# Optimization experiments

Hardware: AMD Instinct MI355X
Metric: run time of the kernel (lower is better)

Reference implementation:

```python
import jax, jax.numpy as jnp
import numpy as np

B, H, W, DIM, WS, SHIFT, HEADS = 32, 56, 56, 256, 7, 3, 8
N = WS * WS          # 49 tokens per window
C2 = 2 * DIM         # concatenated two-modal channel dim
NW = (H // WS) * (W // WS)


def _rel_index(ws):
    coords = np.stack(np.meshgrid(np.arange(ws), np.arange(ws), indexing='ij')).reshape(2, -1)
    rel = (coords[:, :, None] - coords[:, None, :]).transpose(1, 2, 0)
    rel[:, :, 0] += ws - 1
    rel[:, :, 1] += ws - 1
    rel[:, :, 0] *= 2 * ws - 1
    return rel.sum(-1)  # (N, N) int

REL_IDX = _rel_index(WS).reshape(-1)


def _attn_mask():
    # standard Swin shifted-window mask: 0 / -100 per window pair
    img = np.zeros((H, W))
    cnt = 0
    for hs in (slice(0, H - WS), slice(H - WS, H - SHIFT), slice(H - SHIFT, H)):
        for ws_ in (slice(0, W - WS), slice(W - WS, W - SHIFT), slice(W - SHIFT, W)):
            img[hs, ws_] = cnt
            cnt += 1
    mw = img.reshape(H // WS, WS, W // WS, WS).transpose(0, 2, 1, 3).reshape(-1, N)
    d = mw[:, None, :] - mw[:, :, None]
    return np.where(d != 0, -100.0, 0.0).astype(np.float32)  # (nW, N, N)

ATTN_MASK = _attn_mask()


def _win_part(x):  # (B,H,W,C) -> (nW*B, N, C)
    b, c = x.shape[0], x.shape[-1]
    x = x.reshape(b, H // WS, WS, W // WS, WS, c).transpose(0, 1, 3, 2, 4, 5)
    return x.reshape(-1, N, c)


def _win_rev(w, b):  # (nW*B, N, C) -> (B,H,W,C)
    c = w.shape[-1]
    x = w.reshape(b, H // WS, W // WS, WS, WS, c).transpose(0, 1, 3, 2, 4, 5)
    return x.reshape(b, H, W, c)


def _ln(t, g, bb):
    m = t.mean(-1, keepdims=True)
    v = t.var(-1, keepdims=True)
    return (t - m) / jnp.sqrt(v + 1e-5) * g + bb


def setup_inputs() -> dict:
    key = jax.random.key(0)
    ks = jax.random.split(key, 8)
    def nrm(k, shape, s=0.02):
        return jax.random.normal(k, shape, jnp.float32) * s
    return {
        'x': jax.random.normal(ks[0], (B, H * W, DIM), jnp.float32),
        'y': jax.random.normal(ks[1], (B, H * W, DIM), jnp.float32),
        'g1': jnp.ones((DIM,), jnp.float32), 'b1': jnp.zeros((DIM,), jnp.float32),
        'rpb': nrm(ks[2], ((2 * WS - 1) * (2 * WS - 1), HEADS)),
        'w_qkv': nrm(ks[3], (6 * DIM, 2 * DIM)), 'b_qkv': jnp.zeros((6 * DIM,), jnp.float32),
        'w_proj': nrm(ks[4], (DIM, 2 * DIM)), 'b_proj': jnp.zeros((DIM,), jnp.float32),
        'g2': jnp.ones((DIM,), jnp.float32), 'b2': jnp.zeros((DIM,), jnp.float32),
        'w_fc1': nrm(ks[5], (4 * DIM, DIM)), 'b_fc1': jnp.zeros((4 * DIM,), jnp.float32),
        'w_fc2': nrm(ks[6], (DIM, 4 * DIM)), 'b_fc2': jnp.zeros((DIM,), jnp.float32),
    }


def reference(x, y, g1, b1, rpb, w_qkv, b_qkv, w_proj, b_proj, g2, b2, w_fc1, b_fc1, w_fc2, b_fc2):
    scale = (DIM // HEADS) ** -0.5  # as in __init__: head_dim = dim // num_heads
    shortcut = x
    xn = _ln(x, g1, b1).reshape(B, H, W, DIM)
    yn = _ln(y, g1, b1).reshape(B, H, W, DIM)
    # cyclic shift
    xn = jnp.roll(xn, (-SHIFT, -SHIFT), axis=(1, 2))
    yn = jnp.roll(yn, (-SHIFT, -SHIFT), axis=(1, 2))
    xw, yw = _win_part(xn), _win_part(yn)            # (nW*B, N, C)
    xy = jnp.concatenate([xw, yw], axis=-1)          # (nW*B, N, 2C)
    nwb, hd = xy.shape[0], C2 // HEADS
    qkv = (xy @ w_qkv.T + b_qkv).reshape(nwb, N, 3, HEADS, hd).transpose(2, 0, 3, 1, 4)
    q, k, v = qkv[0] * scale, qkv[1], qkv[2]         # (nW*B, h, N, d)
    attn = jnp.einsum('whnd,whmd->whnm', q, k)
    bias = rpb[REL_IDX].reshape(N, N, HEADS).transpose(2, 0, 1)  # (h, N, N)
    attn = attn + bias[None]
    attn = attn.reshape(B, NW, HEADS, N, N) + jnp.asarray(ATTN_MASK)[None, :, None]
    attn = jax.nn.softmax(attn.reshape(nwb, HEADS, N, N), axis=-1)
    out = jnp.einsum('whnm,whmd->whnd', attn, v).transpose(0, 2, 1, 3).reshape(nwb, N, C2)
    out = out @ w_proj.T + b_proj                    # fuse 2C -> C
    out = _win_rev(out, B)
    out = jnp.roll(out, (SHIFT, SHIFT), axis=(1, 2)).reshape(B, H * W, DIM)
    x = shortcut + out
    h = _ln(x, g2, b2)
    h = jax.nn.gelu(h @ w_fc1.T + b_fc1, approximate=False)
    return x + h @ w_fc2.T + b_fc2
```

## Files before the change

kernel.cpp:

```cpp
#include <hip/hip_runtime.h>
#include <hip/hip_bf16.h>

#define DEVI __device__ __forceinline__

typedef __attribute__((ext_vector_type(8))) short short8;
typedef __attribute__((ext_vector_type(4))) float f32x4;
typedef unsigned int u32;
typedef unsigned short u16;

typedef __attribute__((address_space(1))) const u32 gu32_t;
typedef __attribute__((address_space(3))) u32 lu32_t;

DEVI u16 f2bf(float f) {
  u32 u = __builtin_bit_cast(u32, f);
  u32 r = (u + 0x7fffu + ((u >> 16) & 1u)) >> 16;
  return (u16)r;
}

DEVI f32x4 mfma16(short8 a, short8 b, f32x4 c) {
  return __builtin_amdgcn_mfma_f32_16x16x32_bf16(a, b, c, 0, 0, 0);
}

DEVI void gload16(const void* g, void* l) {
  __builtin_amdgcn_global_load_lds((gu32_t*)g, (lu32_t*)l, 16, 0, 0);
}

DEVI float gelu_t(float v) {
  const float u = v * (0.7978845608f + 0.0356774081f * v * v);
  const float t = 1.0f - 2.0f / (__expf(2.0f * u) + 1.0f);
  return 0.5f * v * (1.0f + t);
}

#define CHUNK_ROWS 25088
#define PLANE ((size_t)CHUNK_ROWS * 64)
#define KOFF  ((size_t)8 * PLANE)
#define VOFF  ((size_t)16 * PLANE)

__global__ __launch_bounds__(256) void convk(const float* __restrict__ s, u16* __restrict__ d, int n4) {
  int i = blockIdx.x * 256 + threadIdx.x;
  if (i < n4) {
    const float4 v = ((const float4*)s)[i];
    ushort4 o;
    o.x = f2bf(v.x); o.y = f2bf(v.y); o.z = f2bf(v.z); o.w = f2bf(v.w);
    ((ushort4*)d)[i] = o;
  }
}

__global__ __launch_bounds__(256) void btab_build(const float* __restrict__ rpb, float* __restrict__ btab) {
  const int cls = blockIdx.x >> 3, h = blockIdx.x & 7;
  float* dst = btab + (size_t)(cls * 8 + h) * 4096;
  for (int e = threadIdx.x; e < 4096; e += 256) {
    const int n = e >> 6, m = e & 63;
    float v;
    if (m >= 49) {
      v = -1e30f;
    } else if (n >= 49) {
      v = 0.f;
    } else {
      const int r1 = n / 7, c1 = n - r1 * 7;
      const int r2 = m / 7, c2 = m - r2 * 7;
      const int rel = (r1 - r2 + 6) * 13 + (c1 - c2 + 6);
      v = rpb[rel * 8 + h];
      const int reg1 = ((cls & 1) ? (r1 < 4 ? 1 : 2) : 0) * 3 + ((cls & 2) ? (c1 < 4 ? 1 : 2) : 0);
      const int reg2 = ((cls & 1) ? (r2 < 4 ? 1 : 2) : 0) * 3 + ((cls & 2) ? (c2 < 4 ? 1 : 2) : 0);
      if (reg1 != reg2) v -= 100.f;
    }
    dst[e] = v;
  }
}

__global__ __launch_bounds__(256) void ln_gather(
    const float* __restrict__ x, const float* __restrict__ y,
    const float* __restrict__ g1, const float* __restrict__ b1,
    u16* __restrict__ XY, int rowbase)
{
  const int wv = threadIdx.x >> 6, lane = threadIdx.x & 63;
  const int rl = blockIdx.x * 4 + wv;
  const int row = rowbase + rl;
  const int w = row / 49, n = row - w * 49;
  const int b = w >> 6, win = w & 63, wh = win >> 3, ww = win & 7;
  const int r = n / 7, c = n - r * 7;
  int oh = wh * 7 + r + 3; if (oh >= 56) oh -= 56;
  int ow = ww * 7 + c + 3; if (ow >= 56) ow -= 56;
  const size_t po = ((size_t)b * 3136 + oh * 56 + ow) * 256;
  const float4 g1v = ((const float4*)g1)[lane];
  const float4 b1v = ((const float4*)b1)[lane];
  u16* orow = XY + (size_t)rl * 512;
  #pragma unroll
  for (int mod = 0; mod < 2; ++mod) {
    const float* src = (mod ? y : x) + po;
    const float4 v = ((const float4*)src)[lane];
    float s = v.x + v.y + v.z + v.w;
    #pragma unroll
    for (int off = 1; off < 64; off <<= 1) s += __shfl_xor(s, off);
    const float mean = s * (1.0f / 256.0f);
    const float d0 = v.x - mean, d1 = v.y - mean, d2 = v.z - mean, d3 = v.w - mean;
    float sq = d0 * d0 + d1 * d1 + d2 * d2 + d3 * d3;
    #pragma unroll
    for (int off = 1; off < 64; off <<= 1) sq += __shfl_xor(sq, off);
    const float rstd = rsqrtf(sq * (1.0f / 256.0f) + 1e-5f);
    ushort4 o;
    o.x = f2bf(d0 * rstd * g1v.x + b1v.x);
    o.y = f2bf(d1 * rstd * g1v.y + b1v.y);
    o.z = f2bf(d2 * rstd * g1v.z + b1v.z);
    o.w = f2bf(d3 * rstd * g1v.w + b1v.w);
    *(ushort4*)(orow + mod * 256 + lane * 4) = o;
  }
}

__global__ __launch_bounds__(256) void qkv_gemm(
    const u16* __restrict__ A, const u16* __restrict__ Bw,
    const float* __restrict__ bias, u16* __restrict__ Qo)
{
  __shared__ __align__(16) u16 sA[128 * 64];
  __shared__ __align__(16) u16 sB[128 * 64];
  const int nx = gridDim.x;
  const int nwg = nx * gridDim.y;
  const int orig = blockIdx.y * nx + blockIdx.x;
  const int sw = (orig & 7) * (nwg >> 3) + (orig >> 3);
  const int m0  = (sw / nx) * 128;
  const int nn0 = (sw % nx) * 128;
  const int tid = threadIdx.x;
  const int lane = tid & 63;
  const int wv = tid >> 6;
  const int wm = wv >> 1, wn = wv & 1;
  const int rq = lane & 15, kg = lane >> 4;
  f32x4 acc[4][4];
  #pragma unroll
  for (int i = 0; i < 4; ++i)
    #pragma unroll
    for (int j = 0; j < 4; ++j) acc[i][j] = f32x4{0,0,0,0};

  for (int kt = 0; kt < 8; ++kt) {
    if (kt) __syncthreads();
    #pragma unroll
    for (int i = 0; i < 4; ++i) {
      const int c = i * 256 + tid;
      gload16(A + (size_t)(m0 + (c >> 3)) * 512 + kt * 64 + (c & 7) * 8, sA + c * 8);
    }
    #pragma unroll
    for (int i = 0; i < 4; ++i) {
      const int c = i * 256 + tid;
      gload16(Bw + (size_t)(nn0 + (c >> 3)) * 512 + kt * 64 + (c & 7) * 8, sB + c * 8);
    }
    __syncthreads();
    #pragma unroll
    for (int k0 = 0; k0 < 2; ++k0) {
      short8 af[4], bf8[4];
      #pragma unroll
      for (int mt = 0; mt < 4; ++mt)
        af[mt] = *(const short8*)(sA + (wm * 64 + mt * 16 + rq) * 64 + k0 * 32 + kg * 8);
      #pragma unroll
      for (int nt = 0; nt < 4; ++nt)
        bf8[nt] = *(const short8*)(sB + (wn * 64 + nt * 16 + rq) * 64 + k0 * 32 + kg * 8);
      #pragma unroll
      for (int mt = 0; mt < 4; ++mt)
        #pragma unroll
        for (int nt = 0; nt < 4; ++nt)
          acc[mt][nt] = mfma16(af[mt], bf8[nt], acc[mt][nt]);
    }
  }
  #pragma unroll
  for (int mt = 0; mt < 4; ++mt) {
    #pragma unroll
    for (int nt = 0; nt < 4; ++nt) {
      const int col = nn0 + wn * 64 + nt * 16 + rq;
      const int t = col >> 9, rem = col & 511;
      const int h = rem >> 6, d = rem & 63;
      const float bc = bias[col];
      const float sc = (t == 0) ? 0.17677669529663687f : 1.0f;
      u16* bp = Qo + (size_t)(t * 8 + h) * PLANE + d;
      #pragma unroll
      for (int r = 0; r < 4; ++r) {
        const int row = m0 + wm * 64 + mt * 16 + kg * 4 + r;
        bp[(size_t)row * 64] = f2bf((acc[mt][nt][r] + bc) * sc);
      }
    }
  }
}

__global__ __launch_bounds__(256, 3) void attn3(
    const u16* __restrict__ qkv, const float* __restrict__ btab,
    u16* __restrict__ concat, int wbase)
{
  __shared__ __align__(16) u16 sP[4][3136];
  __shared__ __align__(16) u16 sVT[4][4608];

  const int tid = threadIdx.x;
  const int wv = tid >> 6, lane = tid & 63;
  const int rq = lane & 15, kg = lane >> 4;
  const int gw = blockIdx.x * 4 + wv;
  const int wl = gw >> 3, h = gw & 7;
  const int w = wbase + wl;
  const int win = w & 63, wh = win >> 3, ww = win & 7;
  const int cls = ((wh == 7) ? 1 : 0) | ((ww == 7) ? 2 : 0);
  const float* Tb = btab + (size_t)(cls * 8 + h) * 4096;
  u16* sPw = sP[wv];
  u16* sVw = sVT[wv];

  const u16* qbase = qkv + (size_t)h * PLANE + (size_t)wl * 49 * 64;
  const u16* kbase = qkv + KOFF + (size_t)h * PLANE + (size_t)wl * 49 * 64;
  const u16* vbase = qkv + VOFF + (size_t)h * PLANE + (size_t)wl * 49 * 64;

  short8 vreg[4][2];
  #pragma unroll
  for (int t = 0; t < 4; ++t)
    #pragma unroll
    for (int h2 = 0; h2 < 2; ++h2)
      vreg[t][h2] = *(const short8*)(vbase + (size_t)(16 * t + rq) * 64 + kg * 8 + h2 * 32);

  short8 ak[4][2];
  #pragma unroll
  for (int j = 0; j < 4; ++j) {
    const int rr = (16 * j + rq) > 48 ? 48 : (16 * j + rq);
    ak[j][0] = *(const short8*)(kbase + rr * 64 + kg * 8);
    ak[j][1] = *(const short8*)(kbase + rr * 64 + 32 + kg * 8);
  }
  f32x4 sacc[4][4];
  #pragma unroll
  for (int i = 0; i < 4; ++i)
    #pragma unroll
    for (int j = 0; j < 4; ++j) sacc[i][j] = f32x4{0,0,0,0};
  #pragma unroll
  for (int i = 0; i < 4; ++i) {
    const int rr = (16 * i + rq) > 48 ? 48 : (16 * i + rq);
    const short8 a0 = *(const short8*)(qbase + rr * 64 + kg * 8);
    const short8 a1 = *(const short8*)(qbase + rr * 64 + 32 + kg * 8);
    #pragma unroll
    for (int j = 0; j < 4; ++j) {
      sacc[i][j] = mfma16(a0, ak[j][0], sacc[i][j]);
      sacc[i][j] = mfma16(a1, ak[j][1], sacc[i][j]);
    }
  }

  #pragma unroll
  for (int t = 0; t < 4; ++t) {
    const int row = 16 * t + rq;
    #pragma unroll
    for (int h2 = 0; h2 < 2; ++h2) {
      const int c0 = kg * 8 + h2 * 32;
      #pragma unroll
      for (int j = 0; j < 8; ++j)
        sVw[(c0 + j) * 72 + (row ^ (kg << 4))] = (u16)vreg[t][h2][j];
    }
  }

  #pragma unroll
  for (int i = 0; i < 4; ++i) {
    #pragma unroll
    for (int r = 0; r < 4; ++r) {
      const int n = 16 * i + kg * 4 + r;
      const float* Trow = Tb + n * 64 + rq;
      float pv[4];
      #pragma unroll
      for (int j = 0; j < 4; ++j)
        pv[j] = sacc[i][j][r] + Trow[16 * j];
      float mx = fmaxf(fmaxf(pv[0], pv[1]), fmaxf(pv[2], pv[3]));
      #pragma unroll
      for (int off = 1; off < 16; off <<= 1) mx = fmaxf(mx, __shfl_xor(mx, off));
      float sm = 0.f;
      #pragma unroll
      for (int j = 0; j < 4; ++j) { const float e = __expf(pv[j] - mx); pv[j] = e; sm += e; }
      #pragma unroll
      for (int off = 1; off < 16; off <<= 1) sm += __shfl_xor(sm, off);
      const float inv = 1.0f / sm;
      if (n < 49) {
        #pragma unroll
        for (int j = 0; j < 4; ++j) {
          const int col = 16 * j + rq;
          sPw[n * 64 + (((col >> 3) ^ (n & 7)) << 3) + (col & 7)] = f2bf(pv[j] * inv);
        }
      }
    }
  }

  f32x4 oacc[4][4];
  #pragma unroll
  for (int i = 0; i < 4; ++i)
    #pragma unroll
    for (int j = 0; j < 4; ++j) oacc[i][j] = f32x4{0,0,0,0};
  #pragma unroll
  for (int m0v = 0; m0v < 2; ++m0v) {
    short8 av[4];
    #pragma unroll
    for (int ct = 0; ct < 4; ++ct) {
      const int col = ct * 16 + rq;
      const int s = (col >> 3) & 3;
      short8 vvv = *(const short8*)(sVw + col * 72 + ((m0v * 32 + kg * 8) ^ (s << 4)));
      if (m0v == 1) {
        if (kg == 3) {
          #pragma unroll
          for (int e = 0; e < 8; ++e) vvv[e] = 0;
        } else if (kg == 2) {
          #pragma unroll
          for (int e = 1; e < 8; ++e) vvv[e] = 0;
        }
      }
      av[ct] = vvv;
    }
    #pragma unroll
    for (int i = 0; i < 4; ++i) {
      const int rr = (16 * i + rq) > 48 ? 48 : (16 * i + rq);
      const int ch = (m0v * 4 + kg) ^ (rr & 7);
      const short8 pa = *(const short8*)(sPw + rr * 64 + ch * 8);
      #pragma unroll
      for (int ct = 0; ct < 4; ++ct)
        oacc[i][ct] = mfma16(pa, av[ct], oacc[i][ct]);
    }
  }

  __builtin_amdgcn_s_waitcnt(0);
  #pragma unroll
  for (int i = 0; i < 4; ++i)
    #pragma unroll
    for (int ct = 0; ct < 4; ++ct)
      #pragma unroll
      for (int r = 0; r < 4; ++r) {
        const int n = 16 * i + kg * 4 + r;
        if (n < 49) {
          const int col = ct * 16 + rq;
          sPw[n * 64 + (((col >> 3) ^ (n & 7)) << 3) + (col & 7)] = f2bf(oacc[i][ct][r]);
        }
      }
  u16* crow = concat + (size_t)(wl * 49) * 512 + h * 64;
  #pragma unroll
  for (int it = 0; it < 7; ++it) {
    const int c = it * 64 + lane;
    if (c < 392) {
      const int m = c >> 3, s = c & 7;
      const short8 vvv = *(const short8*)(sPw + m * 64 + ((s ^ (m & 7)) << 3));
      *(short8*)(crow + (size_t)m * 512 + s * 8) = vvv;
    }
  }
}

__global__ __launch_bounds__(256, 2) void projln(
    const u16* __restrict__ A, const u16* __restrict__ Bw,
    const float* __restrict__ bias, const float* __restrict__ x,
    const float* __restrict__ g2, const float* __restrict__ b2,
    float* __restrict__ out, u16* __restrict__ xn2, int rowbase)
{
  __shared__ __align__(16) u16 sA[128 * 64];
  __shared__ __align__(16) u16 sB[256 * 64];
  const int m0 = blockIdx.x * 128;
  const int tid = threadIdx.x;
  const int lane = tid & 63;
  const int wv = tid >> 6;
  const int rq = lane & 15, kg = lane >> 4;
  f32x4 acc[2][16];
  #pragma unroll
  for (int i = 0; i < 2; ++i)
    #pragma unroll
    for (int j = 0; j < 16; ++j) acc[i][j] = f32x4{0,0,0,0};

  for (int kt = 0; kt < 8; ++kt) {
    if (kt) __syncthreads();
    #pragma unroll
    for (int i = 0; i < 4; ++i) {
      const int c = i * 256 + tid;
      gload16(A + (size_t)(m0 + (c >> 3)) * 512 + kt * 64 + (c & 7) * 8, sA + c * 8);
    }
    #pragma unroll
    for (int i = 0; i < 8; ++i) {
      const int c = i * 256 + tid;
      gload16(Bw + (size_t)(c >> 3) * 512 + kt * 64 + (c & 7) * 8, sB + c * 8);
    }
    __syncthreads();
    #pragma unroll
    for (int k0 = 0; k0 < 2; ++k0) {
      short8 af[2];
      #pragma unroll
      for (int mt = 0; mt < 2; ++mt)
        af[mt] = *(const short8*)(sA + (wv * 32 + mt * 16 + rq) * 64 + k0 * 32 + kg * 8);
      #pragma unroll
      for (int nt = 0; nt < 16; ++nt) {
        const short8 bf8 = *(const short8*)(sB + (nt * 16 + rq) * 64 + k0 * 32 + kg * 8);
        #pragma unroll
        for (int mt = 0; mt < 2; ++mt)
          acc[mt][nt] = mfma16(af[mt], bf8, acc[mt][nt]);
      }
    }
  }

  float br[16], g2r[16], b2r[16];
  #pragma unroll
  for (int nt = 0; nt < 16; ++nt) {
    const int col = nt * 16 + rq;
    br[nt] = bias[col]; g2r[nt] = g2[col]; b2r[nt] = b2[col];
  }
  #pragma unroll
  for (int mt = 0; mt < 2; ++mt) {
    #pragma unroll
    for (int r = 0; r < 4; ++r) {
      const int row = m0 + wv * 32 + mt * 16 + kg * 4 + r;
      const u32 g = (u32)(rowbase + row);
      const u32 w = g / 49u; const u32 n = g - w * 49u;
      const int b = w >> 6, win = w & 63, wh = win >> 3, ww = win & 7;
      const u32 rr = n / 7u; const u32 cc = n - rr * 7u;
      int oh = wh * 7 + (int)rr + 3; if (oh >= 56) oh -= 56;
      int ow = ww * 7 + (int)cc + 3; if (ow >= 56) ow -= 56;
      const size_t po = ((size_t)b * 3136 + oh * 56 + ow) * 256;
      float vals[16];
      float s = 0.f;
      #pragma unroll
      for (int nt = 0; nt < 16; ++nt) {
        const float v = acc[mt][nt][r] + br[nt] + x[po + nt * 16 + rq];
        vals[nt] = v; s += v;
      }
      #pragma unroll
      for (int off = 1; off < 16; off <<= 1) s += __shfl_xor(s, off);
      const float mean = s * (1.0f / 256.0f);
      float sq = 0.f;
      #pragma unroll
      for (int nt = 0; nt < 16; ++nt) { const float d_ = vals[nt] - mean; sq += d_ * d_; }
      #pragma unroll
      for (int off = 1; off < 16; off <<= 1) sq += __shfl_xor(sq, off);
      const float rstd = rsqrtf(sq * (1.0f / 256.0f) + 1e-5f);
      #pragma unroll
      for (int nt = 0; nt < 16; ++nt) {
        const int col = nt * 16 + rq;
        out[po + col] = vals[nt];
        xn2[po + col] = f2bf((vals[nt] - mean) * rstd * g2r[nt] + b2r[nt]);
      }
    }
  }
}

__global__ __launch_bounds__(256, 3) void fused_mlp(
    const u16* __restrict__ xn2, const u16* __restrict__ w1,
    const float* __restrict__ bf1, const u16* __restrict__ w2,
    const float* __restrict__ bf2v, float* __restrict__ out)
{
  __shared__ __align__(16) u16 sX[64 * 256];
  __shared__ __align__(16) u16 sH[64 * 128];

  const int m0 = blockIdx.x * 64;
  const int tid = threadIdx.x;
  const int wv = tid >> 6, lane = tid & 63;
  const int rq = lane & 15, kg = lane >> 4;

  #pragma unroll
  for (int i = 0; i < 8; ++i) {
    const int c = i * 256 + tid;
    const int row = c >> 5, ch = c & 31;
    const int sch = (ch & 24) | ((ch ^ row) & 7);
    gload16(xn2 + (size_t)(m0 + row) * 256 + sch * 8, sX + c * 8);
  }

  f32x4 acc2[4][4];
  #pragma unroll
  for (int i = 0; i < 4; ++i)
    #pragma unroll
    for (int j = 0; j < 4; ++j) acc2[i][j] = f32x4{0,0,0,0};

  __syncthreads();

  for (int t = 0; t < 8; ++t) {
    f32x4 a1[4][2];
    #pragma unroll
    for (int i = 0; i < 4; ++i)
      #pragma unroll
      for (int j = 0; j < 2; ++j) a1[i][j] = f32x4{0,0,0,0};
    #pragma unroll
    for (int ks = 0; ks < 8; ++ks) {
      short8 bfr[2];
      #pragma unroll
      for (int nt = 0; nt < 2; ++nt)
        bfr[nt] = *(const short8*)(w1 + (size_t)(t * 128 + wv * 32 + nt * 16 + rq) * 256 + ks * 32 + kg * 8);
      #pragma unroll
      for (int mt = 0; mt < 4; ++mt) {
        const int R = mt * 16 + rq;
        const int wk = ks * 4 + kg;
        const short8 af = *(const short8*)(sX + R * 256 + ((wk & 24) | ((wk ^ R) & 7)) * 8);
        #pragma unroll
        for (int nt = 0; nt < 2; ++nt)
          a1[mt][nt] = mfma16(af, bfr[nt], a1[mt][nt]);
      }
    }
    __syncthreads();
    #pragma unroll
    for (int nt = 0; nt < 2; ++nt) {
      const int col = wv * 32 + nt * 16 + rq;
      const float bb = bf1[t * 128 + col];
      const int ch = col >> 3;
      #pragma unroll
      for (int mt = 0; mt < 4; ++mt)
        #pragma unroll
        for (int r = 0; r < 4; ++r) {
          const int row = mt * 16 + kg * 4 + r;
          sH[row * 128 + ((ch & 8) | ((ch ^ row) & 7)) * 8 + (col & 7)] =
              f2bf(gelu_t(a1[mt][nt][r] + bb));
        }
    }
    __syncthreads();
    #pragma unroll
    for (int ks = 0; ks < 4; ++ks) {
      short8 bfr2[4];
      #pragma unroll
      for (int nt = 0; nt < 4; ++nt)
        bfr2[nt] = *(const short8*)(w2 + (size_t)(wv * 64 + nt * 16 + rq) * 1024 + t * 128 + ks * 32 + kg * 8);
      #pragma unroll
      for (int mt = 0; mt < 4; ++mt) {
        const int R = mt * 16 + rq;
        const int wk = ks * 4 + kg;
        const short8 af = *(const short8*)(sH + R * 128 + ((wk & 8) | ((wk ^ R) & 7)) * 8);
        #pragma unroll
        for (int nt = 0; nt < 4; ++nt)
          acc2[mt][nt] = mfma16(af, bfr2[nt], acc2[mt][nt]);
      }
    }
  }

  #pragma unroll
  for (int nt = 0; nt < 4; ++nt) {
    const int col = wv * 64 + nt * 16 + rq;
    const float bb = bf2v[col];
    #pragma unroll
    for (int mt = 0; mt < 4; ++mt)
      #pragma unroll
      for (int r = 0; r < 4; ++r) {
        float* p = out + (size_t)(m0 + mt * 16 + kg * 4 + r) * 256 + col;
        *p = acc2[mt][nt][r] + bb + *p;
      }
  }
}

extern "C" void kernel_launch(void* const* d_in, const int* in_sizes, int n_in,
                              void* d_out, int out_size, void* d_ws, size_t ws_size,
                              hipStream_t stream) {
  const float* x      = (const float*)d_in[0];
  const float* y      = (const float*)d_in[1];
  const float* g1     = (const float*)d_in[2];
  const float* b1     = (const float*)d_in[3];
  const float* rpb    = (const float*)d_in[4];
  const float* w_qkv  = (const float*)d_in[5];
  const float* b_qkv  = (const float*)d_in[6];
  const float* w_proj = (const float*)d_in[7];
  const float* b_proj = (const float*)d_in[8];
  const float* g2     = (const float*)d_in[9];
  const float* b2     = (const float*)d_in[10];
  const float* w_fc1  = (const float*)d_in[11];
  const float* b_fc1  = (const float*)d_in[12];
  const float* w_fc2  = (const float*)d_in[13];
  const float* b_fc2  = (const float*)d_in[14];
  float* out = (float*)d_out;

  u16* wsp = (u16*)d_ws;
  u16* wqkv_bf  = wsp;
  u16* wproj_bf = wsp + 786432;
  u16* wfc1_bf  = wsp + 917504;
  u16* wfc2_bf  = wsp + 1179648;
  float* btab   = (float*)(wsp + 1441792);
  u16* xn2      = wsp + 1703936;
  u16* XYc      = wsp + 27394048;
  u16* qkvc     = wsp + 40239104;

  convk<<<768, 256, 0, stream>>>(w_qkv,  wqkv_bf,  196608);
  convk<<<128, 256, 0, stream>>>(w_proj, wproj_bf, 32768);
  convk<<<256, 256, 0, stream>>>(w_fc1,  wfc1_bf,  65536);
  convk<<<256, 256, 0, stream>>>(w_fc2,  wfc2_bf,  65536);
  btab_build<<<32, 256, 0, stream>>>(rpb, btab);

  for (int c = 0; c < 4; ++c) {
    ln_gather<<<6272, 256, 0, stream>>>(x, y, g1, b1, XYc, c * CHUNK_ROWS);
    qkv_gemm<<<dim3(12, 196), 256, 0, stream>>>(XYc, wqkv_bf, b_qkv, qkvc);
    attn3<<<1024, 256, 0, stream>>>(qkvc, btab, XYc, c * 512);
    projln<<<196, 256, 0, stream>>>(XYc, wproj_bf, b_proj, x, g2, b2, out, xn2, c * CHUNK_ROWS);
  }

  fused_mlp<<<1568, 256, 0, stream>>>(xn2, wfc1_bf, b_fc1, wfc2_bf, b_fc2, out);
}
```

Measured before the change: 866.2 us.

## Stage QKV epilogue through LDS, shrink attention/proj blocks, merge weight casts

The QKV GEMM epilogue now writes the tile into swizzled shared memory and then emits 16-byte coalesced stores per head plane, replacing scattered 2-byte stores. The attention kernel drops from 4 to 2 waves per block and doubles the grid. The proj+LN kernel uses 64-row tiles with 392 blocks and occupancy hint 3 to fill more CUs. The four weight conversion launches are merged into one. Together these aim to cut uncoalesced write traffic and the tail from too few blocks, at the cost of an extra sync and LDS round trip in the GEMM, and less B-tile reuse in projln.

New measurement: 843.3 us, median of 2. -2.6%, faster.

```diff
diff --git a/kernel.cpp b/kernel.cpp
--- a/kernel.cpp
+++ b/kernel.cpp
@@ -36,14 +36,21 @@
 #define KOFF  ((size_t)8 * PLANE)
 #define VOFF  ((size_t)16 * PLANE)
 
-__global__ __launch_bounds__(256) void convk(const float* __restrict__ s, u16* __restrict__ d, int n4) {
-  int i = blockIdx.x * 256 + threadIdx.x;
-  if (i < n4) {
-    const float4 v = ((const float4*)s)[i];
-    ushort4 o;
-    o.x = f2bf(v.x); o.y = f2bf(v.y); o.z = f2bf(v.z); o.w = f2bf(v.w);
-    ((ushort4*)d)[i] = o;
-  }
+__global__ __launch_bounds__(256) void convall(
+    const float* __restrict__ wq, const float* __restrict__ wp,
+    const float* __restrict__ w1, const float* __restrict__ w2,
+    u16* __restrict__ dq, u16* __restrict__ dp, u16* __restrict__ d1, u16* __restrict__ d2)
+{
+  const int i = blockIdx.x * 256 + threadIdx.x;
+  const float* s; u16* d; int off;
+  if (i < 196608)      { s = wq; d = dq; off = i; }
+  else if (i < 229376) { s = wp; d = dp; off = i - 196608; }
+  else if (i < 294912) { s = w1; d = d1; off = i - 229376; }
+  else                 { s = w2; d = d2; off = i - 294912; }
+  const float4 v = ((const float4*)s)[off];
+  ushort4 o;
+  o.x = f2bf(v.x); o.y = f2bf(v.y); o.z = f2bf(v.z); o.w = f2bf(v.w);
+  ((ushort4*)d)[off] = o;
 }
 
 __global__ __launch_bounds__(256) void btab_build(const float* __restrict__ rpb, float* __restrict__ btab) {
@@ -112,8 +119,9 @@
     const u16* __restrict__ A, const u16* __restrict__ Bw,
     const float* __restrict__ bias, u16* __restrict__ Qo)
 {
-  __shared__ __align__(16) u16 sA[128 * 64];
-  __shared__ __align__(16) u16 sB[128 * 64];
+  __shared__ __align__(16) u16 smem[128 * 128];
+  u16* sA = smem;
+  u16* sB = smem + 128 * 64;
   const int nx = gridDim.x;
   const int nwg = nx * gridDim.y;
   const int orig = blockIdx.y * nx + blockIdx.x;
@@ -160,36 +168,47 @@
           acc[mt][nt] = mfma16(af[mt], bf8[nt], acc[mt][nt]);
     }
   }
-  #pragma unroll
-  for (int mt = 0; mt < 4; ++mt) {
-    #pragma unroll
-    for (int nt = 0; nt < 4; ++nt) {
-      const int col = nn0 + wn * 64 + nt * 16 + rq;
-      const int t = col >> 9, rem = col & 511;
-      const int h = rem >> 6, d = rem & 63;
-      const float bc = bias[col];
-      const float sc = (t == 0) ? 0.17677669529663687f : 1.0f;
-      u16* bp = Qo + (size_t)(t * 8 + h) * PLANE + d;
+  __syncthreads();
+  const int t = nn0 >> 9;
+  const int hbase = (nn0 & 511) >> 6;
+  const float sc = (t == 0) ? 0.17677669529663687f : 1.0f;
+  #pragma unroll
+  for (int nt = 0; nt < 4; ++nt) {
+    const int col = wn * 64 + nt * 16 + rq;
+    const float bc = bias[nn0 + col];
+    const int c = col >> 3;
+    #pragma unroll
+    for (int mt = 0; mt < 4; ++mt)
       #pragma unroll
       for (int r = 0; r < 4; ++r) {
-        const int row = m0 + wm * 64 + mt * 16 + kg * 4 + r;
-        bp[(size_t)row * 64] = f2bf((acc[mt][nt][r] + bc) * sc);
-      }
-    }
-  }
-}
-
-__global__ __launch_bounds__(256, 3) void attn3(
+        const int row = wm * 64 + mt * 16 + kg * 4 + r;
+        smem[row * 128 + (((c & 8) | ((c ^ row) & 7)) << 3) + (col & 7)] =
+            f2bf((acc[mt][nt][r] + bc) * sc);
+      }
+  }
+  __syncthreads();
+  #pragma unroll
+  for (int it = 0; it < 8; ++it) {
+    const int cc = it * 256 + tid;
+    const int row = cc >> 4, c = cc & 15;
+    const int col = c * 8;
+    const int hh = col >> 6, d = col & 63;
+    const short8 v = *(const short8*)(smem + row * 128 + (((c & 8) | ((c ^ row) & 7)) << 3));
+    *(short8*)(Qo + (size_t)(t * 8 + hbase + hh) * PLANE + (size_t)(m0 + row) * 64 + d) = v;
+  }
+}
+
+__global__ __launch_bounds__(128, 3) void attn3(
     const u16* __restrict__ qkv, const float* __restrict__ btab,
     u16* __restrict__ concat, int wbase)
 {
-  __shared__ __align__(16) u16 sP[4][3136];
-  __shared__ __align__(16) u16 sVT[4][4608];
+  __shared__ __align__(16) u16 sP[2][3136];
+  __shared__ __align__(16) u16 sVT[2][4608];
 
   const int tid = threadIdx.x;
   const int wv = tid >> 6, lane = tid & 63;
   const int rq = lane & 15, kg = lane >> 4;
-  const int gw = blockIdx.x * 4 + wv;
+  const int gw = blockIdx.x * 2 + wv;
   const int wl = gw >> 3, h = gw & 7;
   const int w = wbase + wl;
   const int win = w & 63, wh = win >> 3, ww = win & 7;
@@ -334,29 +353,27 @@
   }
 }
 
-__global__ __launch_bounds__(256, 2) void projln(
+__global__ __launch_bounds__(256, 3) void projln(
     const u16* __restrict__ A, const u16* __restrict__ Bw,
     const float* __restrict__ bias, const float* __restrict__ x,
     const float* __restrict__ g2, const float* __restrict__ b2,
     float* __restrict__ out, u16* __restrict__ xn2, int rowbase)
 {
-  __shared__ __align__(16) u16 sA[128 * 64];
+  __shared__ __align__(16) u16 sA[64 * 64];
   __shared__ __align__(16) u16 sB[256 * 64];
-  const int m0 = blockIdx.x * 128;
+  const int m0 = blockIdx.x * 64;
   const int tid = threadIdx.x;
   const int lane = tid & 63;
   const int wv = tid >> 6;
   const int rq = lane & 15, kg = lane >> 4;
-  f32x4 acc[2][16];
-  #pragma unroll
-  for (int i = 0; i < 2; ++i)
-    #pragma unroll
-    for (int j = 0; j < 16; ++j) acc[i][j] = f32x4{0,0,0,0};
+  f32x4 acc[16];
+  #pragma unroll
+  for (int j = 0; j < 16; ++j) acc[j] = f32x4{0,0,0,0};
 
   for (int kt = 0; kt < 8; ++kt) {
     if (kt) __syncthreads();
     #pragma unroll
-    for (int i = 0; i < 4; ++i) {
+    for (int i = 0; i < 2; ++i) {
       const int c = i * 256 + tid;
       gload16(A + (size_t)(m0 + (c >> 3)) * 512 + kt * 64 + (c & 7) * 8, sA + c * 8);
     }
@@ -368,16 +385,11 @@
     __syncthreads();
     #pragma unroll
     for (int k0 = 0; k0 < 2; ++k0) {
-      short8 af[2];
-      #pragma unroll
-      for (int mt = 0; mt < 2; ++mt)
-        af[mt] = *(const short8*)(sA + (wv * 32 + mt * 16 + rq) * 64 + k0 * 32 + kg * 8);
+      const short8 af = *(const short8*)(sA + (wv * 16 + rq) * 64 + k0 * 32 + kg * 8);
       #pragma unroll
       for (int nt = 0; nt < 16; ++nt) {
         const short8 bf8 = *(const short8*)(sB + (nt * 16 + rq) * 64 + k0 * 32 + kg * 8);
-        #pragma unroll
-        for (int mt = 0; mt < 2; ++mt)
-          acc[mt][nt] = mfma16(af[mt], bf8, acc[mt][nt]);
+        acc[nt] = mfma16(af, bf8, acc[nt]);
       }
     }
   }
@@ -389,39 +401,36 @@
     br[nt] = bias[col]; g2r[nt] = g2[col]; b2r[nt] = b2[col];
   }
   #pragma unroll
-  for (int mt = 0; mt < 2; ++mt) {
-    #pragma unroll
-    for (int r = 0; r < 4; ++r) {
-      const int row = m0 + wv * 32 + mt * 16 + kg * 4 + r;
-      const u32 g = (u32)(rowbase + row);
-      const u32 w = g / 49u; const u32 n = g - w * 49u;
-      const int b = w >> 6, win = w & 63, wh = win >> 3, ww = win & 7;
-      const u32 rr = n / 7u; const u32 cc = n - rr * 7u;
-      int oh = wh * 7 + (int)rr + 3; if (oh >= 56) oh -= 56;
-      int ow = ww * 7 + (int)cc + 3; if (ow >= 56) ow -= 56;
-      const size_t po = ((size_t)b * 3136 + oh * 56 + ow) * 256;
-      float vals[16];
-      float s = 0.f;
-      #pragma unroll
-      for (int nt = 0; nt < 16; ++nt) {
-        const float v = acc[mt][nt][r] + br[nt] + x[po + nt * 16 + rq];
-        vals[nt] = v; s += v;
-      }
-      #pragma unroll
-      for (int off = 1; off < 16; off <<= 1) s += __shfl_xor(s, off);
-      const float mean = s * (1.0f / 256.0f);
-      float sq = 0.f;
-      #pragma unroll
-      for (int nt = 0; nt < 16; ++nt) { const float d_ = vals[nt] - mean; sq += d_ * d_; }
-      #pragma unroll
-      for (int off = 1; off < 16; off <<= 1) sq += __shfl_xor(sq, off);
-      const float rstd = rsqrtf(sq * (1.0f / 256.0f) + 1e-5f);
-      #pragma unroll
-      for (int nt = 0; nt < 16; ++nt) {
-        const int col = nt * 16 + rq;
-        out[po + col] = vals[nt];
-        xn2[po + col] = f2bf((vals[nt] - mean) * rstd * g2r[nt] + b2r[nt]);
-      }
+  for (int r = 0; r < 4; ++r) {
+    const int row = m0 + wv * 16 + kg * 4 + r;
+    const u32 g = (u32)(rowbase + row);
+    const u32 w = g / 49u; const u32 n = g - w * 49u;
+    const int b = w >> 6, win = w & 63, wh = win >> 3, ww = win & 7;
+    const u32 rr = n / 7u; const u32 cc = n - rr * 7u;
+    int oh = wh * 7 + (int)rr + 3; if (oh >= 56) oh -= 56;
+    int ow = ww * 7 + (int)cc + 3; if (ow >= 56) ow -= 56;
+    const size_t po = ((size_t)b * 3136 + oh * 56 + ow) * 256;
+    float vals[16];
+    float s = 0.f;
+    #pragma unroll
+    for (int nt = 0; nt < 16; ++nt) {
+      const float v = acc[nt][r] + br[nt] + x[po + nt * 16 + rq];
+      vals[nt] = v; s += v;
+    }
+    #pragma unroll
+    for (int off = 1; off < 16; off <<= 1) s += __shfl_xor(s, off);
+    const float mean = s * (1.0f / 256.0f);
+    float sq = 0.f;
+    #pragma unroll
+    for (int nt = 0; nt < 16; ++nt) { const float d_ = vals[nt] - mean; sq += d_ * d_; }
+    #pragma unroll
+    for (int off = 1; off < 16; off <<= 1) sq += __shfl_xor(sq, off);
+    const float rstd = rsqrtf(sq * (1.0f / 256.0f) + 1e-5f);
+    #pragma unroll
+    for (int nt = 0; nt < 16; ++nt) {
+      const int col = nt * 16 + rq;
+      out[po + col] = vals[nt];
+      xn2[po + col] = f2bf((vals[nt] - mean) * rstd * g2r[nt] + b2r[nt]);
     }
   }
 }
@@ -555,17 +564,15 @@
   u16* XYc      = wsp + 27394048;
   u16* qkvc     = wsp + 40239104;
 
-  convk<<<768, 256, 0, stream>>>(w_qkv,  wqkv_bf,  196608);
-  convk<<<128, 256, 0, stream>>>(w_proj, wproj_bf, 32768);
-  convk<<<256, 256, 0, stream>>>(w_fc1,  wfc1_bf,  65536);
-  convk<<<256, 256, 0, stream>>>(w_fc2,  wfc2_bf,  65536);
+  convall<<<1408, 256, 0, stream>>>(w_qkv, w_proj, w_fc1, w_fc2,
+                                    wqkv_bf, wproj_bf, wfc1_bf, wfc2_bf);
   btab_build<<<32, 256, 0, stream>>>(rpb, btab);
 
   for (int c = 0; c < 4; ++c) {
     ln_gather<<<6272, 256, 0, stream>>>(x, y, g1, b1, XYc, c * CHUNK_ROWS);
     qkv_gemm<<<dim3(12, 196), 256, 0, stream>>>(XYc, wqkv_bf, b_qkv, qkvc);
-    attn3<<<1024, 256, 0, stream>>>(qkvc, btab, XYc, c * 512);
-    projln<<<196, 256, 0, stream>>>(XYc, wproj_bf, b_proj, x, g2, b2, out, xn2, c * CHUNK_ROWS);
+    attn3<<<2048, 128, 0, stream>>>(qkvc, btab, XYc, c * 512);
+    projln<<<392, 256, 0, stream>>>(XYc, wproj_bf, b_proj, x, g2, b2, out, xn2, c * CHUNK_ROWS);
   }
 
   fused_mlp<<<1568, 256, 0, stream>>>(xn2, wfc1_bf, b_fc1, wfc2_bf, b_fc2, out);
```
